# Optimization experiments

Measured on AMD Instinct MI355X. Metric: run time of the kernel, lower is better.

Reference implementation:

```python
import jax, jax.numpy as jnp
import numpy as np

L = 32        # label_num = len(label2idx)
SOS = 0       # label2idx['[SOS]']
END = 1       # label2idx['[END]']
NEG = -10000.0
B, T = 512, 1024


def setup_inputs() -> dict:
    key = jax.random.key(0)
    k1, k2, k3 = jax.random.split(key, 3)
    emission = jax.random.normal(k1, (B, T, L), dtype=jnp.float32)
    label_ids = jax.random.randint(k2, (B, T), 0, L)
    transitions = jax.random.normal(k3, (L, L), dtype=jnp.float32)
    # CrfLayer.__init__: forbid transitions into [SOS] and out of [END]
    transitions = transitions.at[SOS, :].set(NEG).at[:, END].set(NEG)
    return {"emission": emission, "label_ids": label_ids, "transitions": transitions}


def reference(emission, label_ids, transitions):
    b, t, l = emission.shape
    # ---- _forward_alg: log-partition via sequential logsumexp recurrence ----
    alpha0 = jnp.full((b, l), NEG, dtype=emission.dtype).at[:, SOS].set(0.0)
    feats_t = jnp.transpose(emission, (1, 0, 2))  # [T, B, L]

    def step(alpha, feat):
        # aa[b, j, i] = alpha[b, i] + feat[b, j] + transitions[j, i]
        aa = alpha[:, None, :] + feat[:, :, None] + transitions[None, :, :]
        return jax.nn.logsumexp(aa, axis=2), None

    alpha, _ = jax.lax.scan(step, alpha0, feats_t)
    forward_score = jax.nn.logsumexp(alpha + transitions[END][None, :], axis=1)  # [B]

    # ---- _score_sentence: score of the gold path ----
    tags = jnp.concatenate(
        [jnp.full((b, 1), SOS, dtype=label_ids.dtype), label_ids], axis=1)  # [B, T+1]
    trans_score = transitions[tags[:, 1:], tags[:, :-1]].sum(axis=1)          # [B]
    emit_score = jnp.take_along_axis(
        emission, tags[:, 1:, None].astype(jnp.int32), axis=2)[..., 0].sum(axis=1)  # [B]
    gold_score = trans_score + emit_score + transitions[END, tags[:, -1]]

    # loss = sum(forward_score - gold_score)
    return jnp.sum(forward_score - gold_score)
```

## Files before the change

### kernel.cpp

```cpp
#include <hip/hip_runtime.h>


typedef float  f32x16 __attribute__((ext_vector_type(16)));
typedef short  s16x8  __attribute__((ext_vector_type(8)));
typedef float  f32x2  __attribute__((ext_vector_type(2)));

#define TT 1024
#define LL 32
#define BB 512
#define NC 8
#define CL 128
#define MS 33

union Frag { s16x8 v; unsigned u[4]; };

__device__ __forceinline__ unsigned pack_bf16(float lo, float hi) {
    return __builtin_amdgcn_perm(__float_as_uint(hi), __float_as_uint(lo), 0x07060302u);
}

__device__ __forceinline__ void skew_sleep(int n) {
    switch (n & 3) {
        case 1: __builtin_amdgcn_s_sleep(1); break;
        case 2: __builtin_amdgcn_s_sleep(2); break;
        case 3: __builtin_amdgcn_s_sleep(3); break;
        default: break;
    }
}

__global__ __launch_bounds__(NC * 64, 4) void crf_fused_kernel(
    const float* __restrict__ emission,
    const int*   __restrict__ label_ids,
    const float* __restrict__ transitions,
    float*       __restrict__ out)
{
    __shared__ __align__(16) float shM[NC][32 * MS];
    __shared__ float shQ[2][64];
    __shared__ float tgArr[NC];
    __shared__ int   capArr[NC];

    const int tid  = threadIdx.x;
    const int w    = tid >> 6;
    const int lane = tid & 63;
    const int j    = lane & 31;
    const int h    = lane >> 5;
    const int b    = blockIdx.x;
    const int t0   = w * CL;

    const int*   labB = label_ids + b * TT + t0;
    const float* emB  = emission + ((size_t)b * TT + t0) * LL + j;

    {
        float g = 0.0f;
#pragma unroll
        for (int u = 0; u < 2; ++u) {
            int tt = t0 + 64 * u + lane;
            int l1 = labB[64 * u + lane];
            int l0 = (tt == 0) ? 0 : label_ids[b * TT + tt - 1];
            g += transitions[(l1 << 5) + l0];
            g += emission[((size_t)b * TT + tt) * LL + l1];
            if (tt == TT - 1) g += transitions[32 + l1];
        }
#pragma unroll
        for (int m = 32; m >= 1; m >>= 1) g += __shfl_xor(g, m, 64);
        if (lane == 0) tgArr[w] = g;
    }

    const float* trow = transitions + j * 32;
    f32x2 E0v[4], E1v[4];
#pragma unroll
    for (int p = 0; p < 4; ++p) {
        int c0 = ((2 * p) & 3)     + 8 * ((2 * p) >> 2)     + 4 * h;
        int c1 = ((2 * p + 1) & 3) + 8 * ((2 * p + 1) >> 2) + 4 * h;
        E0v[p][0] = __expf(trow[c0]);      E0v[p][1] = __expf(trow[c1]);
        E1v[p][0] = __expf(trow[16 + c0]); E1v[p][1] = __expf(trow[16 + c1]);
    }

    Frag B0, B1;
#pragma unroll
    for (int i = 0; i < 8; ++i) {
        int row = (i & 3) + 8 * (i >> 2) + 4 * h;
        B0.v[i] = (short)((row == j)      ? 0x3F80 : 0);
        B1.v[i] = (short)((row + 16 == j) ? 0x3F80 : 0);
    }

    f32x16 zc, acc;
#pragma unroll
    for (int i = 0; i < 16; ++i) zc[i] = 0.0f;

    float ring[8];
#pragma unroll
    for (int s = 0; s < 8; ++s) ring[s] = emB[s * LL];

    float sc = 1.0f;
    int   Cap = 0, elast = 0;

    skew_sleep(w + ((blockIdx.x & 1) << 1));

    auto step = [&](int k, int s, bool refill) {
        float feat = ring[k];
        float fs = ((k & 3) == 0) ? (__expf(feat) * sc) : __expf(feat);
        f32x2 fs2; fs2[0] = fs; fs2[1] = fs;

        Frag A0, A1;
#pragma unroll
        for (int p = 0; p < 4; ++p) {
            f32x2 a = fs2 * E0v[p];
            f32x2 c = fs2 * E1v[p];
            A0.u[p] = pack_bf16(a[0], a[1]);
            A1.u[p] = pack_bf16(c[0], c[1]);
        }

        acc = __builtin_amdgcn_mfma_f32_32x32x16_bf16(A0.v, B0.v, zc, 0, 0, 0);
        acc = __builtin_amdgcn_mfma_f32_32x32x16_bf16(A1.v, B1.v, acc, 0, 0, 0);

        if ((k & 3) == 3) {
            int pb = __builtin_amdgcn_readlane(__float_as_int(acc[2]), 0);
            int e  = ((pb >> 23) & 0xff) - 127;
            sc = __int_as_float((127 - e) << 23);
            Cap += e;
            elast = e;
        }

        if (refill) ring[k] = emB[(s + 8) * LL];

#pragma unroll
        for (int p = 0; p < 4; ++p) {
            B0.u[p] = pack_bf16(acc[2 * p],     acc[2 * p + 1]);
            B1.u[p] = pack_bf16(acc[8 + 2 * p], acc[9 + 2 * p]);
        }
    };

    for (int s0 = 0; s0 < CL - 8; s0 += 8) {
#pragma unroll
        for (int k = 0; k < 8; ++k) step(k, s0 + k, true);
    }
#pragma unroll
    for (int k = 0; k < 8; ++k) step(k, CL - 8 + k, false);

    Cap -= elast;

#pragma unroll
    for (int r = 0; r < 16; ++r) {
        int row = (r & 3) + 8 * (r >> 2) + 4 * h;
        shM[w][row * MS + j] = acc[r];
    }
    if (lane == 0) capArr[w] = Cap;

    __syncthreads();

    if (w == 0) {
        const float Eend = __expf(transitions[32 + j]);
        float q = (j == 0) ? 1.0f : 0.0f;
        int   Cq = 0;
        float gold = 0.0f;

#pragma unroll
        for (int c = 0; c < NC; ++c) {
            shQ[c & 1][lane] = q;
            asm volatile("s_waitcnt lgkmcnt(0)" ::: "memory");
            __builtin_amdgcn_wave_barrier();
            const float* Mrow = &shM[c][j * MS];
            const float* qv   = &shQ[c & 1][h * 32];
            float a0 = 0.f, a1 = 0.f, a2 = 0.f, a3 = 0.f;
#pragma unroll
            for (int i = 0; i < 32; i += 4) {
                a0 = fmaf(Mrow[i],     qv[i],     a0);
                a1 = fmaf(Mrow[i + 1], qv[i + 1], a1);
                a2 = fmaf(Mrow[i + 2], qv[i + 2], a2);
                a3 = fmaf(Mrow[i + 3], qv[i + 3], a3);
            }
            float qn = (a0 + a1) + (a2 + a3);
            int pb = __builtin_amdgcn_readlane(__float_as_int(qn), 2);
            int e  = ((pb >> 23) & 0xff) - 127;
            qn *= __int_as_float((127 - e) << 23);
            Cq += e + capArr[c];
            gold += tgArr[c];
            q = qn;
        }

        float v = q * Eend;
#pragma unroll
        for (int m = 16; m >= 1; m >>= 1) v += __shfl_xor(v, m, 32);
        float fwd = __logf(v) + (float)Cq * 0.69314718055994531f;

        if (lane == 0) atomicAdd(out, fwd - gold);
    }
}

extern "C" void kernel_launch(void* const* d_in, const int* in_sizes, int n_in,
                              void* d_out, int out_size, void* d_ws, size_t ws_size,
                              hipStream_t stream)
{
    const float* emission    = (const float*)d_in[0];
    const int*   label_ids   = (const int*)d_in[1];
    const float* transitions = (const float*)d_in[2];
    float* out = (float*)d_out;

    (void)hipMemsetAsync(out, 0, sizeof(float), stream);
    crf_fused_kernel<<<BB, NC * 64, 0, stream>>>(emission, label_ids, transitions, out);
}
```

Measured before the change: 136.4 us.

## Split each sequence into 16 chunks of 64 steps per block

Doubles the waves per block from 8 to 16, so each wave runs a 64-step chained MFMA recurrence instead of 128, halving the serial critical path. Shared memory for the chunk matrices is reused in two phases: wave 0 combines the first 8 chunk products, then the remaining 8 waves write theirs and wave 0 combines again. This adds two extra block barriers and a longer serial combine in wave 0, and requires more waves resident per CU at the launch bound of 8.

```diff
diff --git a/kernel.cpp b/kernel.cpp
--- a/kernel.cpp
+++ b/kernel.cpp
@@ -8,8 +8,9 @@
 #define TT 1024
 #define LL 32
 #define BB 512
-#define NC 8
-#define CL 128
+#define NW 16
+#define CL 64
+#define NCH 8
 #define MS 33
 
 union Frag { s16x8 v; unsigned u[4]; };
@@ -27,16 +28,16 @@
     }
 }
 
-__global__ __launch_bounds__(NC * 64, 4) void crf_fused_kernel(
+__global__ __launch_bounds__(NW * 64, 8) void crf_fused_kernel(
     const float* __restrict__ emission,
     const int*   __restrict__ label_ids,
     const float* __restrict__ transitions,
     float*       __restrict__ out)
 {
-    __shared__ __align__(16) float shM[NC][32 * MS];
+    __shared__ __align__(16) float shM[NCH][32 * MS];
     __shared__ float shQ[2][64];
-    __shared__ float tgArr[NC];
-    __shared__ int   capArr[NC];
+    __shared__ float tgArr[NW];
+    __shared__ int   capArr[NW];
 
     const int tid  = threadIdx.x;
     const int w    = tid >> 6;
@@ -51,15 +52,12 @@
 
     {
         float g = 0.0f;
-#pragma unroll
-        for (int u = 0; u < 2; ++u) {
-            int tt = t0 + 64 * u + lane;
-            int l1 = labB[64 * u + lane];
-            int l0 = (tt == 0) ? 0 : label_ids[b * TT + tt - 1];
-            g += transitions[(l1 << 5) + l0];
-            g += emission[((size_t)b * TT + tt) * LL + l1];
-            if (tt == TT - 1) g += transitions[32 + l1];
-        }
+        int tt = t0 + lane;
+        int l1 = labB[lane];
+        int l0 = (tt == 0) ? 0 : label_ids[b * TT + tt - 1];
+        g += transitions[(l1 << 5) + l0];
+        g += emission[((size_t)b * TT + tt) * LL + l1];
+        if (tt == TT - 1) g += transitions[32 + l1];
 #pragma unroll
         for (int m = 32; m >= 1; m >>= 1) g += __shfl_xor(g, m, 64);
         if (lane == 0) tgArr[w] = g;
@@ -94,7 +92,7 @@
     float sc = 1.0f;
     int   Cap = 0, elast = 0;
 
-    skew_sleep(w + ((blockIdx.x & 1) << 1));
+    skew_sleep((w >> 2) + ((blockIdx.x & 1) << 1));
 
     auto step = [&](int k, int s, bool refill) {
         float feat = ring[k];
@@ -139,23 +137,24 @@
 
     Cap -= elast;
 
-#pragma unroll
-    for (int r = 0; r < 16; ++r) {
-        int row = (r & 3) + 8 * (r >> 2) + 4 * h;
-        shM[w][row * MS + j] = acc[r];
-    }
     if (lane == 0) capArr[w] = Cap;
 
-    __syncthreads();
-
-    if (w == 0) {
-        const float Eend = __expf(transitions[32 + j]);
-        float q = (j == 0) ? 1.0f : 0.0f;
-        int   Cq = 0;
-        float gold = 0.0f;
-
-#pragma unroll
-        for (int c = 0; c < NC; ++c) {
+    if (w < NCH) {
+#pragma unroll
+        for (int r = 0; r < 16; ++r) {
+            int row = (r & 3) + 8 * (r >> 2) + 4 * h;
+            shM[w][row * MS + j] = acc[r];
+        }
+    }
+
+    const float Eend = __expf(transitions[32 + j]);
+    float q    = (j == 0) ? 1.0f : 0.0f;
+    int   Cq   = 0;
+    float gold = 0.0f;
+
+    auto combine8 = [&](int base) {
+#pragma unroll
+        for (int c = 0; c < NCH; ++c) {
             shQ[c & 1][lane] = q;
             asm volatile("s_waitcnt lgkmcnt(0)" ::: "memory");
             __builtin_amdgcn_wave_barrier();
@@ -173,10 +172,30 @@
             int pb = __builtin_amdgcn_readlane(__float_as_int(qn), 2);
             int e  = ((pb >> 23) & 0xff) - 127;
             qn *= __int_as_float((127 - e) << 23);
-            Cq += e + capArr[c];
-            gold += tgArr[c];
+            Cq += e + capArr[base + c];
+            gold += tgArr[base + c];
             q = qn;
         }
+    };
+
+    __syncthreads();
+
+    if (w == 0) combine8(0);
+
+    __syncthreads();
+
+    if (w >= NCH) {
+#pragma unroll
+        for (int r = 0; r < 16; ++r) {
+            int row = (r & 3) + 8 * (r >> 2) + 4 * h;
+            shM[w - NCH][row * MS + j] = acc[r];
+        }
+    }
+
+    __syncthreads();
+
+    if (w == 0) {
+        combine8(NCH);
 
         float v = q * Eend;
 #pragma unroll
@@ -197,5 +216,5 @@
     float* out = (float*)d_out;
 
     (void)hipMemsetAsync(out, 0, sizeof(float), stream);
-    crf_fused_kernel<<<BB, NC * 64, 0, stream>>>(emission, label_ids, transitions, out);
-}
+    crf_fused_kernel<<<BB, NW * 64, 0, stream>>>(emission, label_ids, transitions, out);
+}
```

Result: slower. 146.9 us (+7.7%).
